# Kernel tuning notes

Measured on AMD Instinct MI355X. Metric: run time of the kernel, lower is better.

## Reference

```python
import jax, jax.numpy as jnp
import numpy as np

B, H_WIN, W_WIN = 2048, 8, 8
N = H_WIN * W_WIN            # tokens per window = 64
C = 384                      # channels
HEADS, HEAD_DIM = 12, 32
E = HEADS * HEAD_DIM         # embedding channels = 384
EPS = 1e-5


def _relative_position_indices(h, w):
    coords = np.stack(np.meshgrid(np.arange(h), np.arange(w), indexing='ij')).reshape(2, -1)  # [2, N]
    rel = coords[:, :, None] - coords[:, None, :]      # [2, N, N]
    rel = rel.transpose(1, 2, 0).astype(np.int64)      # [N, N, 2]
    rel[..., 0] = (rel[..., 0] + h - 1) * (2 * w - 1)
    rel[..., 1] += w - 1
    return rel.sum(-1)                                 # [N, N] in [0, (2h-1)(2w-1))


def setup_inputs() -> dict:
    key = jax.random.key(0)
    ks = jax.random.split(key, 6)
    x = jax.random.normal(ks[0], (B, N, C), dtype=jnp.float32)
    ln_g = jnp.ones((C,), jnp.float32)
    ln_b = jnp.zeros((C,), jnp.float32)
    w_qkv = jax.random.normal(ks[1], (3 * E, C), jnp.float32) * (1.0 / np.sqrt(C))
    w_out = jax.random.normal(ks[2], (C, E), jnp.float32) * (1.0 / np.sqrt(E))
    b_out = jnp.zeros((C,), jnp.float32)
    n_bias = (2 * H_WIN - 1) * (2 * W_WIN - 1)
    bias_table = jax.random.truncated_normal(ks[3], -2.0, 2.0, (n_bias, HEADS), jnp.float32) * 0.02
    rel_idx = jnp.asarray(_relative_position_indices(H_WIN, W_WIN))  # [N, N] int64
    return {"x": x, "ln_g": ln_g, "ln_b": ln_b, "w_qkv": w_qkv,
            "w_out": w_out, "b_out": b_out, "bias_table": bias_table, "rel_idx": rel_idx}


def reference(x, ln_g, ln_b, w_qkv, w_out, b_out, bias_table, rel_idx):
    # pre-norm
    mu = jnp.mean(x, axis=-1, keepdims=True)
    var = jnp.var(x, axis=-1, keepdims=True)
    xn = (x - mu) * jax.lax.rsqrt(var + EPS) * ln_g + ln_b
    # qkv projection (no bias)
    qkv = jnp.einsum('bnc,ec->bne', xn, w_qkv)                     # [B, N, 3E]
    qkv = qkv.reshape(x.shape[0], N, 3, HEADS, HEAD_DIM)
    q, k, v = (qkv[:, :, i].transpose(0, 2, 1, 3) for i in range(3))  # each [B, h, N, d]
    scale = 1.0 / np.sqrt(HEAD_DIM)
    scores = jnp.einsum('bhnd,bhmd->bhnm', q * scale, k)           # [B, h, N, N]
    # gather learned relative-position bias per (n, m) pair
    bias = bias_table[rel_idx]                                     # [N, N, h]
    scores = scores + bias.transpose(2, 0, 1)[None]                # broadcast over B
    p = jax.nn.softmax(scores, axis=-1)
    out = jnp.einsum('bhnm,bhmd->bhnd', p, v)                      # [B, h, N, d]
    out = out.transpose(0, 2, 1, 3).reshape(x.shape[0], N, E)
    return jnp.einsum('bne,ce->bnc', out, w_out) + b_out
```

## Files before the change

kernel.cpp:

```cpp
#include <hip/hip_runtime.h>
#include <hip/hip_bf16.h>


#define NTOK  64
#define CCH   384
#define NH    12
#define HD    32
#define EPSV  1e-5f
#define SCALEQ 0.17677669529663687f

#define WQP_ELEMS (72 * 12 * 64 * 8)
#define WOP_ELEMS (24 * 12 * 64 * 8)
#define BLUTP_ELEMS (12 * 4 * 4 * 64 * 4)

typedef __attribute__((ext_vector_type(8))) short  short8;
typedef __attribute__((ext_vector_type(4))) short  short4v;
typedef __attribute__((ext_vector_type(4))) float  float4v;
typedef __attribute__((ext_vector_type(4))) int    int4v;

__device__ __forceinline__ unsigned short f2bf(float f) {
    union { float f; unsigned int i; } v; v.f = f;
    unsigned int r = v.i + 0x7fffu + ((v.i >> 16) & 1u);
    return (unsigned short)(r >> 16);
}
__device__ __forceinline__ unsigned int pack2bf(float lo, float hi) {
    return (unsigned int)f2bf(lo) | ((unsigned int)f2bf(hi) << 16);
}
__device__ __forceinline__ short4v pack4bf(float a, float b, float c, float d) {
    short4v p;
    p[0] = (short)f2bf(a); p[1] = (short)f2bf(b);
    p[2] = (short)f2bf(c); p[3] = (short)f2bf(d);
    return p;
}

__global__ void prep_kernel(const float* __restrict__ w_qkv_f,
                            const float* __restrict__ w_out_f,
                            const float* __restrict__ bias_tab,
                            const int*   __restrict__ rel_idx,
                            unsigned short* __restrict__ wqp,
                            unsigned short* __restrict__ wop,
                            float* __restrict__ blutp) {
    const int stride = gridDim.x * blockDim.x;
    const int tid = blockIdx.x * blockDim.x + threadIdx.x;
    for (int i = tid; i < WQP_ELEMS; i += stride) {
        const int t = i / 6144, rem = i % 6144;
        const int kk = rem >> 9, rem2 = rem & 511;
        const int lane = rem2 >> 3, e = rem2 & 7;
        wqp[i] = f2bf(w_qkv_f[(16 * t + (lane & 15)) * CCH + 32 * kk + 8 * (lane >> 4) + e]);
    }
    for (int i = tid; i < WOP_ELEMS; i += stride) {
        const int t = i / 6144, rem = i % 6144;
        const int kk = rem >> 9, rem2 = rem & 511;
        const int lane = rem2 >> 3, e = rem2 & 7;
        wop[i] = f2bf(w_out_f[(16 * t + (lane & 15)) * CCH + 32 * kk + 8 * (lane >> 4) + e]);
    }
    for (int i = tid; i < BLUTP_ELEMS; i += stride) {
        const int r = i & 3, lane = (i >> 2) & 63;
        const int kt = (i >> 8) & 3, tt = (i >> 10) & 3, h = i >> 12;
        const int token = 16 * tt + (lane & 15);
        const int key   = 16 * kt + 4 * (lane >> 4) + r;
        blutp[i] = bias_tab[rel_idx[token * 64 + key] * NH + h];
    }
}

__global__ __launch_bounds__(512, 2)
void fused_win_mha(const float* __restrict__ x,
                   const float* __restrict__ ln_g,
                   const float* __restrict__ ln_b,
                   const float* __restrict__ b_out,
                   const unsigned short* __restrict__ wqp,
                   const unsigned short* __restrict__ wop,
                   const float* __restrict__ blutp,
                   float* __restrict__ out)
{
    const int b    = blockIdx.x;
    const int t    = threadIdx.x;
    const int wav  = t >> 6;
    const int lane = t & 63;
    const int l4   = lane >> 4;
    const int lc   = lane & 15;
    const int lh   = wav >> 1;
    const int mh   = wav & 1;

    __shared__ unsigned short xnp[4 * 12 * 64 * 8];
    __shared__ unsigned short qp [4 * 4 * 64 * 8];
    __shared__ unsigned short kp [4 * 4 * 64 * 8];
    __shared__ unsigned short vp [2][4 * 2 * 2 * 64 * 8];
    __shared__ unsigned short attp[4 * 4 * 64 * 8];

    {
        const int row = t >> 3, seg = t & 7;
        const float* xr = x + (b * NTOK + row) * CCH + seg * 48;
        float vals[48];
        float s = 0.f, s2 = 0.f;
        #pragma unroll
        for (int i = 0; i < 12; ++i) {
            float4v v = *(const float4v*)(xr + i * 4);
            #pragma unroll
            for (int j = 0; j < 4; ++j) {
                float f = v[j];
                vals[i * 4 + j] = f; s += f; s2 += f * f;
            }
        }
        s += __shfl_xor(s, 1); s2 += __shfl_xor(s2, 1);
        s += __shfl_xor(s, 2); s2 += __shfl_xor(s2, 2);
        s += __shfl_xor(s, 4); s2 += __shfl_xor(s2, 4);
        const float mu   = s * (1.f / CCH);
        const float rstd = rsqrtf(s2 * (1.f / CCH) - mu * mu + EPSV);
        #pragma unroll
        for (int u = 0; u < 6; ++u) {
            const int col0 = seg * 48 + u * 8;
            short8 w;
            #pragma unroll
            for (int e2 = 0; e2 < 2; ++e2) {
                float4v gv = *(const float4v*)(ln_g + col0 + e2 * 4);
                float4v bv = *(const float4v*)(ln_b + col0 + e2 * 4);
                #pragma unroll
                for (int j = 0; j < 4; ++j)
                    w[e2 * 4 + j] = (short)f2bf((vals[u * 8 + e2 * 4 + j] - mu) * rstd * gv[j] + bv[j]);
            }
            const int idx = ((((row >> 4) * 12 + (col0 >> 5)) << 9)
                             + ((((col0 >> 3) & 3) * 16 + (row & 15)) << 3));
            *(short8*)&xnp[idx] = w;
        }
    }
    __syncthreads();

    float4v facc[4][3];
    #pragma unroll
    for (int mt = 0; mt < 4; ++mt)
        #pragma unroll
        for (int j = 0; j < 3; ++j)
            facc[mt][j] = (float4v){0.f, 0.f, 0.f, 0.f};

    float sv[2][4][4];
    float mx[2];
    float4v bbn[2][4];

    #pragma unroll
    for (int it = 0; it < 4; ++it) {
        short8 bGb[4][3];
        if (it > 0) {
            const int g = it - 1;
            #pragma unroll
            for (int ks = 0; ks < 4; ++ks)
                #pragma unroll
                for (int j2 = 0; j2 < 3; ++j2)
                    bGb[ks][j2] = *(const short8*)&wop[(((3 * wav + j2) * 12 + 4 * g + ks) << 9) + (lane << 3)];
        }
        if (it < 3) {
            const int h = 4 * it + lh;
            #pragma unroll
            for (int j = 0; j < 2; ++j)
                #pragma unroll
                for (int kt = 0; kt < 4; ++kt)
                    bbn[j][kt] = *(const float4v*)(blutp + ((((h * 4 + (2 * mh + j)) * 4 + kt) << 6) + lane) * 4);
        }

        short8 af[2][2];
        if (it > 0) {
            unsigned int pk2[2][4][2];
            #pragma unroll
            for (int j = 0; j < 2; ++j) {
                float sk[4];
                #pragma unroll
                for (int kt = 0; kt < 4; ++kt) {
                    float pe0 = __expf(sv[j][kt][0] - mx[j]);
                    float pe1 = __expf(sv[j][kt][1] - mx[j]);
                    float pe2 = __expf(sv[j][kt][2] - mx[j]);
                    float pe3 = __expf(sv[j][kt][3] - mx[j]);
                    sv[j][kt][0] = pe0; sv[j][kt][1] = pe1;
                    sv[j][kt][2] = pe2; sv[j][kt][3] = pe3;
                    sk[kt] = (pe0 + pe1) + (pe2 + pe3);
                }
                float s = (sk[0] + sk[1]) + (sk[2] + sk[3]);
                s += __shfl_xor(s, 16);
                s += __shfl_xor(s, 32);
                const float rinv = 1.f / s;
                #pragma unroll
                for (int kt = 0; kt < 4; ++kt) {
                    pk2[j][kt][0] = pack2bf(sv[j][kt][0] * rinv, sv[j][kt][1] * rinv);
                    pk2[j][kt][1] = pack2bf(sv[j][kt][2] * rinv, sv[j][kt][3] * rinv);
                }
            }
            const int src0 = lc + 16 * (2 * (l4 & 1));
            const int src1 = src0 + 16;
            const bool hi  = ((l4 >> 1) & 1) != 0;
            #pragma unroll
            for (int j = 0; j < 2; ++j) {
                #pragma unroll
                for (int kk2 = 0; kk2 < 2; ++kk2) {
                    const int ka = 2 * kk2, kb = 2 * kk2 + 1;
                    unsigned int a0a = (unsigned int)__shfl((int)pk2[j][ka][0], src0);
                    unsigned int a0b = (unsigned int)__shfl((int)pk2[j][kb][0], src0);
                    unsigned int a1a = (unsigned int)__shfl((int)pk2[j][ka][1], src0);
                    unsigned int a1b = (unsigned int)__shfl((int)pk2[j][kb][1], src0);
                    unsigned int a2a = (unsigned int)__shfl((int)pk2[j][ka][0], src1);
                    unsigned int a2b = (unsigned int)__shfl((int)pk2[j][kb][0], src1);
                    unsigned int a3a = (unsigned int)__shfl((int)pk2[j][ka][1], src1);
                    unsigned int a3b = (unsigned int)__shfl((int)pk2[j][kb][1], src1);
                    int4v iv;
                    iv[0] = (int)(hi ? a0b : a0a);
                    iv[1] = (int)(hi ? a1b : a1a);
                    iv[2] = (int)(hi ? a2b : a2a);
                    iv[3] = (int)(hi ? a3b : a3a);
                    af[j][kk2] = __builtin_bit_cast(short8, iv);
                }
            }
        }

        float4v acc[3][4];
        int tile_[3];
        if (it < 3) {
            const int h = 4 * it + lh;
            #pragma unroll
            for (int n = 0; n < 3; ++n) {
                tile_[n] = n * 24 + h * 2 + mh;
                #pragma unroll
                for (int m = 0; m < 4; ++m)
                    acc[n][m] = (float4v){0.f, 0.f, 0.f, 0.f};
            }
            #pragma unroll
            for (int kk = 0; kk < 12; ++kk) {
                short8 aF[4];
                #pragma unroll
                for (int mt = 0; mt < 4; ++mt)
                    aF[mt] = *(const short8*)&xnp[((mt * 12 + kk) << 9) + (lane << 3)];
                short8 bF0 = *(const short8*)&wqp[((tile_[0] * 12 + kk) << 9) + (lane << 3)];
                short8 bF1 = *(const short8*)&wqp[((tile_[1] * 12 + kk) << 9) + (lane << 3)];
                short8 bF2 = *(const short8*)&wqp[((tile_[2] * 12 + kk) << 9) + (lane << 3)];
                #pragma unroll
                for (int mt = 0; mt < 4; ++mt) {
                    acc[0][mt] = __builtin_amdgcn_mfma_f32_16x16x32_bf16(bF0, aF[mt], acc[0][mt], 0, 0, 0);
                    acc[1][mt] = __builtin_amdgcn_mfma_f32_16x16x32_bf16(bF1, aF[mt], acc[1][mt], 0, 0, 0);
                    acc[2][mt] = __builtin_amdgcn_mfma_f32_16x16x32_bf16(aF[mt], bF2, acc[2][mt], 0, 0, 0);
                }
            }
        }

        if (it > 0) {
            const unsigned short* vpr = vp[(it - 1) & 1];
            float4v o[2][2];
            #pragma unroll
            for (int j = 0; j < 2; ++j)
                #pragma unroll
                for (int nt = 0; nt < 2; ++nt)
                    o[j][nt] = (float4v){0.f, 0.f, 0.f, 0.f};
            #pragma unroll
            for (int kk2 = 0; kk2 < 2; ++kk2) {
                #pragma unroll
                for (int nt = 0; nt < 2; ++nt) {
                    short8 vf = *(const short8*)&vpr[(((lh * 2 + nt) * 2 + kk2) << 9) + (lane << 3)];
                    #pragma unroll
                    for (int j = 0; j < 2; ++j)
                        o[j][nt] = __builtin_amdgcn_mfma_f32_16x16x32_bf16(vf, af[j][kk2], o[j][nt], 0, 0, 0);
                }
            }
            #pragma unroll
            for (int j = 0; j < 2; ++j) {
                #pragma unroll
                for (int nt = 0; nt < 2; ++nt) {
                    const int addr = (((2 * mh + j) * 4 + lh) << 9)
                                   + (((2 * nt + (l4 >> 1)) * 16 + lc) << 3)
                                   + ((l4 & 1) << 2);
                    *(short4v*)&attp[addr] = pack4bf(o[j][nt][0], o[j][nt][1], o[j][nt][2], o[j][nt][3]);
                }
            }
        }

        if (it < 3) {
            unsigned short* vpw = vp[it & 1];
            #pragma unroll
            for (int mt = 0; mt < 4; ++mt) {
                short4v pq, pkk, pv;
                #pragma unroll
                for (int r = 0; r < 4; ++r) {
                    pq[r]  = (short)f2bf(acc[0][mt][r] * SCALEQ);
                    pkk[r] = (short)f2bf(acc[1][mt][r]);
                    pv[r]  = (short)f2bf(acc[2][mt][r]);
                }
                const int aqk = ((lh * 4 + mt) << 9)
                              + (((2 * mh + (l4 >> 1)) * 16 + lc) << 3)
                              + ((l4 & 1) << 2);
                *(short4v*)&qp[aqk] = pq;
                *(short4v*)&kp[aqk] = pkk;
                const int av = (((lh * 2 + mh) * 2 + (mt >> 1)) << 9)
                             + ((((mt & 1) * 2 + (l4 >> 1)) * 16 + lc) << 3)
                             + ((l4 & 1) << 2);
                *(short4v*)&vpw[av] = pv;
            }
        }
        __syncthreads();

        if (it > 0) {
            #pragma unroll
            for (int ks = 0; ks < 4; ++ks) {
                short8 aG[4];
                #pragma unroll
                for (int mt = 0; mt < 4; ++mt)
                    aG[mt] = *(const short8*)&attp[((mt * 4 + ks) << 9) + (lane << 3)];
                #pragma unroll
                for (int j2 = 0; j2 < 3; ++j2)
                    #pragma unroll
                    for (int mt = 0; mt < 4; ++mt)
                        facc[mt][j2] = __builtin_amdgcn_mfma_f32_16x16x32_bf16(aG[mt], bGb[ks][j2], facc[mt][j2], 0, 0, 0);
            }
        }
        if (it < 3) {
            #pragma unroll
            for (int j = 0; j < 2; ++j) {
                short8 qf = *(const short8*)&qp[((lh * 4 + (2 * mh + j)) << 9) + (lane << 3)];
                #pragma unroll
                for (int kt = 0; kt < 4; ++kt) {
                    short8 kf = *(const short8*)&kp[((lh * 4 + kt) << 9) + (lane << 3)];
                    float4v sres = __builtin_amdgcn_mfma_f32_16x16x32_bf16(
                        kf, qf, (float4v){0.f, 0.f, 0.f, 0.f}, 0, 0, 0);
                    #pragma unroll
                    for (int r = 0; r < 4; ++r) sv[j][kt][r] = sres[r];
                }
            }
            #pragma unroll
            for (int j = 0; j < 2; ++j) {
                float m = -1e30f;
                #pragma unroll
                for (int kt = 0; kt < 4; ++kt) {
                    #pragma unroll
                    for (int r = 0; r < 4; ++r) {
                        sv[j][kt][r] += bbn[j][kt][r];
                        m = fmaxf(m, sv[j][kt][r]);
                    }
                }
                m = fmaxf(m, __shfl_xor(m, 16));
                m = fmaxf(m, __shfl_xor(m, 32));
                mx[j] = m;
            }
        }
        __syncthreads();
    }

    {
        float* ob = out + b * (NTOK * CCH);
        #pragma unroll
        for (int mt = 0; mt < 4; ++mt) {
            #pragma unroll
            for (int j2 = 0; j2 < 3; ++j2) {
                const int c = 16 * (3 * wav + j2) + lc;
                const float bo = b_out[c];
                #pragma unroll
                for (int r = 0; r < 4; ++r)
                    ob[(16 * mt + 4 * l4 + r) * CCH + c] = facc[mt][j2][r] + bo;
            }
        }
    }
}

extern "C" void kernel_launch(void* const* d_in, const int* in_sizes, int n_in,
                              void* d_out, int out_size, void* d_ws, size_t ws_size,
                              hipStream_t stream) {
    const float* x     = (const float*)d_in[0];
    const float* ln_g  = (const float*)d_in[1];
    const float* ln_b  = (const float*)d_in[2];
    const float* w_qkv = (const float*)d_in[3];
    const float* w_out = (const float*)d_in[4];
    const float* b_out = (const float*)d_in[5];
    const float* btab  = (const float*)d_in[6];
    const int*   ridx  = (const int*)d_in[7];
    float*       out   = (float*)d_out;

    unsigned short* wqp   = (unsigned short*)d_ws;
    unsigned short* wop   = wqp + WQP_ELEMS;
    float*          blutp = (float*)(wop + WOP_ELEMS);

    prep_kernel<<<512, 256, 0, stream>>>(w_qkv, w_out, btab, ridx, wqp, wop, blutp);
    fused_win_mha<<<2048, 512, 0, stream>>>(x, ln_g, ln_b, b_out, wqp, wop, blutp, out);
}
```

Before: 280.9 us.

## Process two windows per block with a cross-window software pipeline

Each block now handles two windows (bid and bid+1024) in one 7-stage loop, so the head-group pipeline runs on without draining between windows. The second window's layernorm is issued during stage 2, and the first window's epilogue is written at stage 4 before the output accumulators are reset. This removes one pipeline fill/drain per window and halves the grid to 1024 blocks. In exchange the loop is no longer unrolled (runtime g/g2 indexing), register pressure may rise, and fewer blocks can leave CUs underused.

```diff
diff --git a/kernel.cpp b/kernel.cpp
--- a/kernel.cpp
+++ b/kernel.cpp
@@ -73,7 +73,7 @@
                    const float* __restrict__ blutp,
                    float* __restrict__ out)
 {
-    const int b    = blockIdx.x;
+    const int bid  = blockIdx.x;
     const int t    = threadIdx.x;
     const int wav  = t >> 6;
     const int lane = t & 63;
@@ -88,7 +88,12 @@
     __shared__ unsigned short vp [2][4 * 2 * 2 * 64 * 8];
     __shared__ unsigned short attp[4 * 4 * 64 * 8];
 
-    {
+    float4v facc[4][3];
+    float sv[2][4][4];
+    float mx[2];
+    float4v bbn[2][4];
+
+    auto do_ln = [&](int b) {
         const int row = t >> 3, seg = t & 7;
         const float* xr = x + (b * NTOK + row) * CCH + seg * 48;
         float vals[48];
@@ -123,33 +128,53 @@
                              + ((((col0 >> 3) & 3) * 16 + (row & 15)) << 3));
             *(short8*)&xnp[idx] = w;
         }
-    }
+    };
+    auto do_epilogue = [&](int b) {
+        float* ob = out + b * (NTOK * CCH);
+        #pragma unroll
+        for (int mt = 0; mt < 4; ++mt) {
+            #pragma unroll
+            for (int j2 = 0; j2 < 3; ++j2) {
+                const int c = 16 * (3 * wav + j2) + lc;
+                const float bo = b_out[c];
+                #pragma unroll
+                for (int r = 0; r < 4; ++r)
+                    ob[(16 * mt + 4 * l4 + r) * CCH + c] = facc[mt][j2][r] + bo;
+            }
+        }
+    };
+
+    do_ln(bid);
     __syncthreads();
 
-    float4v facc[4][3];
     #pragma unroll
     for (int mt = 0; mt < 4; ++mt)
         #pragma unroll
         for (int j = 0; j < 3; ++j)
             facc[mt][j] = (float4v){0.f, 0.f, 0.f, 0.f};
 
-    float sv[2][4][4];
-    float mx[2];
-    float4v bbn[2][4];
-
-    #pragma unroll
-    for (int it = 0; it < 4; ++it) {
+    for (int u = 0; u <= 6; ++u) {
+        const int g  = u - (u >= 3 ? 3 : 0) - (u >= 6 ? 3 : 0);
+        const int g2 = (u + 2) - ((u + 2) >= 3 ? 3 : 0) - ((u + 2) >= 6 ? 3 : 0);
+
+        if (u == 4) {
+            do_epilogue(bid);
+            #pragma unroll
+            for (int mt = 0; mt < 4; ++mt)
+                #pragma unroll
+                for (int j = 0; j < 3; ++j)
+                    facc[mt][j] = (float4v){0.f, 0.f, 0.f, 0.f};
+        }
         short8 bGb[4][3];
-        if (it > 0) {
-            const int g = it - 1;
+        if (u >= 1) {
             #pragma unroll
             for (int ks = 0; ks < 4; ++ks)
                 #pragma unroll
                 for (int j2 = 0; j2 < 3; ++j2)
-                    bGb[ks][j2] = *(const short8*)&wop[(((3 * wav + j2) * 12 + 4 * g + ks) << 9) + (lane << 3)];
-        }
-        if (it < 3) {
-            const int h = 4 * it + lh;
+                    bGb[ks][j2] = *(const short8*)&wop[(((3 * wav + j2) * 12 + 4 * g2 + ks) << 9) + (lane << 3)];
+        }
+        if (u < 6) {
+            const int h = 4 * g + lh;
             #pragma unroll
             for (int j = 0; j < 2; ++j)
                 #pragma unroll
@@ -158,7 +183,7 @@
         }
 
         short8 af[2][2];
-        if (it > 0) {
+        if (u >= 1) {
             unsigned int pk2[2][4][2];
             #pragma unroll
             for (int j = 0; j < 2; ++j) {
@@ -211,8 +236,8 @@
 
         float4v acc[3][4];
         int tile_[3];
-        if (it < 3) {
-            const int h = 4 * it + lh;
+        if (u < 6) {
+            const int h = 4 * g + lh;
             #pragma unroll
             for (int n = 0; n < 3; ++n) {
                 tile_[n] = n * 24 + h * 2 + mh;
@@ -238,8 +263,8 @@
             }
         }
 
-        if (it > 0) {
-            const unsigned short* vpr = vp[(it - 1) & 1];
+        if (u >= 1) {
+            const unsigned short* vpr = vp[(u - 1) & 1];
             float4v o[2][2];
             #pragma unroll
             for (int j = 0; j < 2; ++j)
@@ -268,8 +293,8 @@
             }
         }
 
-        if (it < 3) {
-            unsigned short* vpw = vp[it & 1];
+        if (u < 6) {
+            unsigned short* vpw = vp[u & 1];
             #pragma unroll
             for (int mt = 0; mt < 4; ++mt) {
                 short4v pq, pkk, pv;
@@ -292,7 +317,7 @@
         }
         __syncthreads();
 
-        if (it > 0) {
+        if (u >= 1) {
             #pragma unroll
             for (int ks = 0; ks < 4; ++ks) {
                 short8 aG[4];
@@ -306,7 +331,7 @@
                         facc[mt][j2] = __builtin_amdgcn_mfma_f32_16x16x32_bf16(aG[mt], bGb[ks][j2], facc[mt][j2], 0, 0, 0);
             }
         }
-        if (it < 3) {
+        if (u < 6) {
             #pragma unroll
             for (int j = 0; j < 2; ++j) {
                 short8 qf = *(const short8*)&qp[((lh * 4 + (2 * mh + j)) << 9) + (lane << 3)];
@@ -335,23 +360,11 @@
                 mx[j] = m;
             }
         }
+        if (u == 2) do_ln(bid + 1024);
         __syncthreads();
     }
 
-    {
-        float* ob = out + b * (NTOK * CCH);
-        #pragma unroll
-        for (int mt = 0; mt < 4; ++mt) {
-            #pragma unroll
-            for (int j2 = 0; j2 < 3; ++j2) {
-                const int c = 16 * (3 * wav + j2) + lc;
-                const float bo = b_out[c];
-                #pragma unroll
-                for (int r = 0; r < 4; ++r)
-                    ob[(16 * mt + 4 * l4 + r) * CCH + c] = facc[mt][j2][r] + bo;
-            }
-        }
-    }
+    do_epilogue(bid + 1024);
 }
 
 extern "C" void kernel_launch(void* const* d_in, const int* in_sizes, int n_in,
@@ -372,5 +385,5 @@
     float*          blutp = (float*)(wop + WOP_ELEMS);
 
     prep_kernel<<<512, 256, 0, stream>>>(w_qkv, w_out, btab, ridx, wqp, wop, blutp);
-    fused_win_mha<<<2048, 512, 0, stream>>>(x, ln_g, ln_b, b_out, wqp, wop, blutp, out);
-}
+    fused_win_mha<<<1024, 512, 0, stream>>>(x, ln_g, ln_b, b_out, wqp, wop, blutp, out);
+}
```

Result: slower. 810.1 us (+188.4%).
